# Performance work log

Hardware: AMD Instinct MI355X
Metric: run time of the kernel (lower is better)

## Reference

```python
import jax, jax.numpy as jnp
import numpy as np

N, E, F, H = 20000, 320000, 128, 256   # nodes, edges, in-features, hidden
M, NQ = 4096, 2048                      # lsq rows, QP variables
LAMB_MAX = 2.0


def setup_inputs() -> dict:
    key = jax.random.key(0)
    ks = jax.random.split(key, 12)
    x = jax.random.normal(ks[0], (N, F), jnp.float32)
    edge_index = jax.random.randint(ks[1], (2, E), 0, N)
    A = jax.random.normal(ks[2], (M, NQ), jnp.float32) * 0.05
    b = jax.random.normal(ks[3], (M, 1), jnp.float32)
    feat_ids = jax.random.randint(ks[4], (NQ,), 0, N)
    x_prior = jax.random.uniform(ks[5], (NQ, 1), jnp.float32)
    lamb = jnp.ones((1,), jnp.float32)
    # ChebConv K=2 weights: one linear per Chebyshev order, plus bias
    W10 = jax.random.normal(ks[6], (F, H), jnp.float32) / np.sqrt(F)
    W11 = jax.random.normal(ks[7], (F, H), jnp.float32) / np.sqrt(F)
    b1 = jnp.zeros((H,), jnp.float32)
    W20 = jax.random.normal(ks[8], (H, 1), jnp.float32) / np.sqrt(H)
    W21 = jax.random.normal(ks[9], (H, 1), jnp.float32) / np.sqrt(H)
    b2 = jnp.zeros((1,), jnp.float32)
    return {"x": x, "edge_index": edge_index, "A": A, "b": b,
            "feat_ids": feat_ids, "x_prior": x_prior, "lamb": lamb,
            "W10": W10, "W11": W11, "b1": b1,
            "W20": W20, "W21": W21, "b2": b2}


def _cheb_conv(x, edge_index, W0, W1, bias, lam_max):
    """PyG ChebConv with K=2: out = x @ W0 + (2L/lam_max - I) x @ W1 + bias,
    L = I - D^{-1/2} A D^{-1/2}, via edge gather/scatter (no dense NxN)."""
    row, col = edge_index[0], edge_index[1]
    n = x.shape[0]
    deg = jax.ops.segment_sum(jnp.ones_like(row, dtype=x.dtype), row, num_segments=n)
    dinv = jnp.where(deg > 0, deg ** -0.5, 0.0)
    # normalized edge weight scaled by 2/lam_max, negated (off-diag of L_hat)
    w = -(2.0 / lam_max) * dinv[row] * dinv[col]              # [E]
    msg = jax.ops.segment_sum(w[:, None] * x[col], row, num_segments=n)
    Tx1 = msg + (2.0 / lam_max - 1.0) * x                      # diagonal of L_hat
    return x @ W0 + Tx1 @ W1 + bias


def reference(x, edge_index, A, b, feat_ids, x_prior, lamb,
              W10, W11, b1, W20, W21, b2):
    h = jax.nn.relu(_cheb_conv(x, edge_index, W10, W11, b1, LAMB_MAX))
    h = lamb[0] * jax.nn.relu(_cheb_conv(h, edge_index, W20, W21, b2, LAMB_MAX))
    hfold = h[feat_ids] + 1e-5                                 # [NQ, 1]
    q = hfold[:, 0]
    # QP: min 1/2 z^T Q z + p^T z with vacuous inequality (0*z <= 0.1) and no
    # equality constraints -> interior-point converges to unconstrained min.
    Q = A.T @ A + jnp.diag(q)                                  # [NQ, NQ]
    p = -(x_prior * hfold)[:, 0] - (b.T @ A)[0]                # [NQ]
    z = jnp.linalg.solve(Q, -p)                                # [NQ]
    return z[:, None]                                          # f.T -> [NQ, 1]
```

## Files before the change

### kernel.cpp

```cpp
#include <hip/hip_runtime.h>

#define N_NODES 20000
#define N_EDGES 320000
#define F_DIM   128
#define H_DIM   256
#define M_ROWS  4096
#define NQ      2048
#define NIT     18
#define MM_ROWS 20032

typedef __attribute__((ext_vector_type(8))) short short8;
typedef __attribute__((ext_vector_type(4))) float f32x4;


__device__ __forceinline__ float wred(float v) {
#pragma unroll
  for (int m = 32; m > 0; m >>= 1) v += __shfl_xor(v, m, 64);
  return v;
}

__device__ __forceinline__ float bred256(float v, float* lds) {
  v = wred(v);
  int w = threadIdx.x >> 6;
  if ((threadIdx.x & 63) == 0) lds[w] = v;
  __syncthreads();
  float tot = lds[0] + lds[1] + lds[2] + lds[3];
  __syncthreads();
  return tot;
}

__device__ __forceinline__ unsigned f2bf(float f) {
  unsigned u = __float_as_uint(f);
  unsigned r = u + 0x7fffu + ((u >> 16) & 1u);
  return r >> 16;
}
__device__ __forceinline__ float bflo(unsigned u) { return __uint_as_float(u << 16); }
__device__ __forceinline__ float bfhi(unsigned u) { return __uint_as_float(u & 0xffff0000u); }


__global__ __launch_bounds__(1024) void k_scan(const int* __restrict__ deg,
    int* __restrict__ rowstart, float* __restrict__ dinv) {
  __shared__ int part[1024];
  int t = threadIdx.x;
  const int chunk = (N_NODES + 1023) / 1024;
  int lo = t * chunk;
  int hi = lo + chunk; if (hi > N_NODES) hi = N_NODES;
  int s = 0;
  for (int i = lo; i < hi; ++i) {
    int d = deg[i];
    dinv[i] = d > 0 ? rsqrtf((float)d) : 0.f;
    s += d;
  }
  part[t] = s;
  __syncthreads();
  for (int off = 1; off < 1024; off <<= 1) {
    int v = part[t];
    int add = (t >= off) ? part[t - off] : 0;
    __syncthreads();
    part[t] = v + add;
    __syncthreads();
  }
  int base = (t > 0) ? part[t - 1] : 0;
  for (int i = lo; i < hi; ++i) { rowstart[i] = base; base += deg[i]; }
  if (t == 0) rowstart[N_NODES] = part[1023];
}

__global__ __launch_bounds__(256) void k_scatter(const int* __restrict__ ei,
    const int* __restrict__ rowstart, int* __restrict__ cursor,
    const float* __restrict__ dinv, int* __restrict__ cols, float* __restrict__ wvals) {
  int e = blockIdx.x * 256 + threadIdx.x;
  if (e >= N_EDGES) return;
  int r = ei[e];
  int c = ei[N_EDGES + e];
  int pos = rowstart[r] + atomicAdd(&cursor[r], 1);
  cols[pos] = c;
  wvals[pos] = -dinv[r] * dinv[c];
}

#define CONVX_BLKS (MM_ROWS * 16 / 256)
#define DEG_BLKS   ((N_EDGES + 255) / 256)

__global__ __launch_bounds__(256) void k_pack(const float* __restrict__ x,
    const float* __restrict__ W10, const float* __restrict__ W11,
    unsigned* __restrict__ xu, unsigned* __restrict__ Wtb,
    const int* __restrict__ ei, int* __restrict__ deg) {
  int bx = blockIdx.x;
  if (bx < CONVX_BLKS) {
    int gid = bx * 256 + threadIdx.x;
    int row = gid >> 4;
    int q8 = gid & 15;
    uint4* xu4 = (uint4*)xu;
    if (row < N_NODES) {
      const float4* x4 = (const float4*)x;
      float4 a = x4[(size_t)row * 32 + q8 * 2];
      float4 b2 = x4[(size_t)row * 32 + q8 * 2 + 1];
      uint4 u;
      u.x = f2bf(a.x) | (f2bf(a.y) << 16);
      u.y = f2bf(a.z) | (f2bf(a.w) << 16);
      u.z = f2bf(b2.x) | (f2bf(b2.y) << 16);
      u.w = f2bf(b2.z) | (f2bf(b2.w) << 16);
      xu4[(size_t)row * 32 + q8] = u;
    } else {
      uint4 z = make_uint4(0, 0, 0, 0);
      xu4[(size_t)row * 32 + q8] = z;
      xu4[(size_t)row * 32 + 16 + q8] = z;
    }
  } else if (bx < CONVX_BLKS + 128) {
    int gid = (bx - CONVX_BLKS) * 256 + threadIdx.x;
    int n = gid >> 7;
    int u = gid & 127;
    int k0 = u * 2;
    float v0 = (k0 < 128) ? W10[(size_t)k0 * H_DIM + n]
                          : W11[(size_t)(k0 - 128) * H_DIM + n];
    float v1 = (k0 + 1 < 128) ? W10[(size_t)(k0 + 1) * H_DIM + n]
                              : W11[(size_t)(k0 - 127) * H_DIM + n];
    Wtb[(size_t)n * 128 + u] = f2bf(v0) | (f2bf(v1) << 16);
  } else {
    int e = (bx - CONVX_BLKS - 128) * 256 + threadIdx.x;
    if (e < N_EDGES) atomicAdd(&deg[ei[e]], 1);
  }
}

#define PT_ST 130

__global__ __launch_bounds__(256) void k_prep2(const float* __restrict__ A,
    const float* __restrict__ b, unsigned* __restrict__ Atu,
    float* __restrict__ btA_parts) {
  __shared__ unsigned short T[64 * PT_ST];
  __shared__ float part[64 * 4];
  const int t = threadIdx.x;
  const int jt = blockIdx.x & 31, kt = blockIdx.x >> 5;
  const int j0 = jt * 64, k0 = kt * 128;
  const int jl = t & 63, kq = t >> 6;
  float bta = 0.f;
#pragma unroll 8
  for (int p = 0; p < 32; ++p) {
    int row = k0 + p * 4 + kq;
    float v = A[(size_t)row * NQ + j0 + jl];
    bta += b[row] * v;
    T[jl * PT_ST + p * 4 + kq] = (unsigned short)f2bf(v);
  }
  part[jl * 4 + kq] = bta;
  __syncthreads();
  const int jr = t >> 2, c = t & 3;
  const unsigned short* Tr = T + jr * PT_ST + c * 32;
  uint4 uu0, uu1, uu2, uu3;
  uu0.x = (unsigned)Tr[0]  | ((unsigned)Tr[1]  << 16);
  uu0.y = (unsigned)Tr[2]  | ((unsigned)Tr[3]  << 16);
  uu0.z = (unsigned)Tr[4]  | ((unsigned)Tr[5]  << 16);
  uu0.w = (unsigned)Tr[6]  | ((unsigned)Tr[7]  << 16);
  uu1.x = (unsigned)Tr[8]  | ((unsigned)Tr[9]  << 16);
  uu1.y = (unsigned)Tr[10] | ((unsigned)Tr[11] << 16);
  uu1.z = (unsigned)Tr[12] | ((unsigned)Tr[13] << 16);
  uu1.w = (unsigned)Tr[14] | ((unsigned)Tr[15] << 16);
  uu2.x = (unsigned)Tr[16] | ((unsigned)Tr[17] << 16);
  uu2.y = (unsigned)Tr[18] | ((unsigned)Tr[19] << 16);
  uu2.z = (unsigned)Tr[20] | ((unsigned)Tr[21] << 16);
  uu2.w = (unsigned)Tr[22] | ((unsigned)Tr[23] << 16);
  uu3.x = (unsigned)Tr[24] | ((unsigned)Tr[25] << 16);
  uu3.y = (unsigned)Tr[26] | ((unsigned)Tr[27] << 16);
  uu3.z = (unsigned)Tr[28] | ((unsigned)Tr[29] << 16);
  uu3.w = (unsigned)Tr[30] | ((unsigned)Tr[31] << 16);
  uint4* dst = (uint4*)(Atu + (size_t)(j0 + jr) * 2048 + kt * 64 + c * 16);
  dst[0] = uu0; dst[1] = uu1; dst[2] = uu2; dst[3] = uu3;
  if (t < 64) {
    float s4 = (part[t * 4] + part[t * 4 + 1]) + (part[t * 4 + 2] + part[t * 4 + 3]);
    btA_parts[(size_t)kt * NQ + j0 + t] = s4;
  }
}

__global__ __launch_bounds__(256) void k_msg1(const int* __restrict__ rowstart,
    const int* __restrict__ cols, const float* __restrict__ wvals,
    unsigned* __restrict__ xu) {
  int wid = (blockIdx.x * 256 + threadIdx.x) >> 6;
  int lane = threadIdx.x & 63;
  if (wid >= N_NODES) return;
  int s0 = rowstart[wid], s1 = rowstart[wid + 1];
  float2 a0 = make_float2(0.f, 0.f), a1 = make_float2(0.f, 0.f);
  float2 a2 = make_float2(0.f, 0.f), a3 = make_float2(0.f, 0.f);
  int e = s0;
  for (; e + 4 <= s1; e += 4) {
    int c0 = cols[e], c1 = cols[e + 1], c2 = cols[e + 2], c3 = cols[e + 3];
    float w0 = wvals[e], w1 = wvals[e + 1], w2 = wvals[e + 2], w3 = wvals[e + 3];
    unsigned u0 = xu[(size_t)c0 * 128 + lane];
    unsigned u1 = xu[(size_t)c1 * 128 + lane];
    unsigned u2 = xu[(size_t)c2 * 128 + lane];
    unsigned u3 = xu[(size_t)c3 * 128 + lane];
    a0.x += w0 * bflo(u0); a0.y += w0 * bfhi(u0);
    a1.x += w1 * bflo(u1); a1.y += w1 * bfhi(u1);
    a2.x += w2 * bflo(u2); a2.y += w2 * bfhi(u2);
    a3.x += w3 * bflo(u3); a3.y += w3 * bfhi(u3);
  }
  for (; e < s1; ++e) {
    int c = cols[e];
    float w = wvals[e];
    unsigned u = xu[(size_t)c * 128 + lane];
    a0.x += w * bflo(u); a0.y += w * bfhi(u);
  }
  float ax = (a0.x + a1.x) + (a2.x + a3.x);
  float ay = (a0.y + a1.y) + (a2.y + a3.y);
  xu[(size_t)wid * 128 + 64 + lane] = f2bf(ax) | (f2bf(ay) << 16);
}


__device__ __forceinline__ void mm_ldfrag(short8* Af, short8* Bf,
    const unsigned* __restrict__ xurow, const unsigned* __restrict__ wrow, int kc) {
#pragma unroll
  for (int a = 0; a < 4; ++a)
    Af[a] = *(const short8*)(xurow + (size_t)a * 16 * 128 + kc * 16);
#pragma unroll
  for (int n = 0; n < 4; ++n)
    Bf[n] = *(const short8*)(wrow + (size_t)n * 16 * 128 + kc * 16);
}

__global__ __launch_bounds__(256) void k_mm(const unsigned* __restrict__ xu,
    const unsigned* __restrict__ Wtb, const float* __restrict__ b1,
    const float* __restrict__ W20, const float* __restrict__ W21,
    float* __restrict__ t, float* __restrict__ s) {
  const int row0 = blockIdx.x * 64;
  const int tid = threadIdx.x;
  const int w = tid >> 6, lane = tid & 63;
  const int colb = w * 64;
  const int frow = lane & 15, fqo = (lane >> 4) * 4;
  const int c16 = lane & 15, q4 = lane >> 4;

  f32x4 acc[4][4];
#pragma unroll
  for (int a = 0; a < 4; ++a)
#pragma unroll
    for (int b = 0; b < 4; ++b) {
      acc[a][b][0] = 0.f; acc[a][b][1] = 0.f;
      acc[a][b][2] = 0.f; acc[a][b][3] = 0.f;
    }

  const unsigned* xurow = xu + (size_t)(row0 + frow) * 128 + fqo;
  const unsigned* wrow  = Wtb + (size_t)(colb + frow) * 128 + fqo;

  short8 A0[4], B0[4], A1[4], B1[4];
  mm_ldfrag(A0, B0, xurow, wrow, 0);
#pragma unroll
  for (int kp = 0; kp < 4; ++kp) {
    const int kc = kp * 2;
    mm_ldfrag(A1, B1, xurow, wrow, kc + 1);
#pragma unroll
    for (int a = 0; a < 4; ++a)
#pragma unroll
      for (int n = 0; n < 4; ++n)
        acc[a][n] = __builtin_amdgcn_mfma_f32_16x16x32_bf16(A0[a], B0[n], acc[a][n], 0, 0, 0);
    if (kc + 2 < 8) mm_ldfrag(A0, B0, xurow, wrow, kc + 2);
#pragma unroll
    for (int a = 0; a < 4; ++a)
#pragma unroll
      for (int n = 0; n < 4; ++n)
        acc[a][n] = __builtin_amdgcn_mfma_f32_16x16x32_bf16(A1[a], B1[n], acc[a][n], 0, 0, 0);
  }

  float tp[4][4] = {}, sp[4][4] = {};
#pragma unroll
  for (int b2 = 0; b2 < 4; ++b2) {
    int gc = colb + b2 * 16 + c16;
    float w20 = W20[gc], w21 = W21[gc], bb = b1[gc];
#pragma unroll
    for (int a = 0; a < 4; ++a)
#pragma unroll
      for (int r = 0; r < 4; ++r) {
        float val = acc[a][b2][r] + bb;
        val = val > 0.f ? val : 0.f;
        tp[a][r] += val * w20;
        sp[a][r] += val * w21;
      }
  }
#pragma unroll
  for (int a = 0; a < 4; ++a)
#pragma unroll
    for (int r = 0; r < 4; ++r) {
#pragma unroll
      for (int m = 1; m < 16; m <<= 1) {
        tp[a][r] += __shfl_xor(tp[a][r], m, 64);
        sp[a][r] += __shfl_xor(sp[a][r], m, 64);
      }
    }
  if (c16 == 0) {
#pragma unroll
    for (int a = 0; a < 4; ++a)
#pragma unroll
      for (int r = 0; r < 4; ++r) {
        int gr = row0 + a * 16 + q4 * 4 + r;
        if (gr < N_NODES) {
          atomicAdd(&t[gr], tp[a][r]);
          atomicAdd(&s[gr], sp[a][r]);
        }
      }
  }
}


__global__ __launch_bounds__(256) void k_h2(const float* __restrict__ t,
    const float* __restrict__ s, const int* __restrict__ rowstart,
    const int* __restrict__ cols, const float* __restrict__ wvals,
    const float* __restrict__ lamb, const float* __restrict__ b2, float* __restrict__ h2) {
  int i = blockIdx.x * 256 + threadIdx.x;
  if (i >= N_NODES) return;
  int s0 = rowstart[i], s1 = rowstart[i + 1];
  float m0 = 0.f, m1 = 0.f, m2 = 0.f, m3 = 0.f;
  int e = s0;
  for (; e + 4 <= s1; e += 4) {
    int c0 = cols[e], c1 = cols[e + 1], c2 = cols[e + 2], c3 = cols[e + 3];
    float w0 = wvals[e], w1 = wvals[e + 1], w2 = wvals[e + 2], w3 = wvals[e + 3];
    m0 += w0 * s[c0];
    m1 += w1 * s[c1];
    m2 += w2 * s[c2];
    m3 += w3 * s[c3];
  }
  for (; e < s1; ++e) m0 += wvals[e] * s[cols[e]];
  float m = (m0 + m1) + (m2 + m3);
  float val = t[i] + m + b2[0];
  val = val > 0.f ? val : 0.f;
  h2[i] = lamb[0] * val;
}

#define GR_ST2 36
#define NTILE 136

__global__ __launch_bounds__(512) void k_gram(const unsigned* __restrict__ Atu,
    float* __restrict__ Gp,
    const float* __restrict__ h2, const int* __restrict__ feat_ids,
    const float* __restrict__ x_prior, const float* __restrict__ btA_parts,
    float* __restrict__ q, float* __restrict__ r0) {
  if (blockIdx.x >= 544) {
    if (threadIdx.x < 256) {
      int j = (blockIdx.x - 544) * 256 + threadIdx.x;
      int f = feat_ids[j];
      float hf = h2[f] + 1e-5f;
      q[j] = hf;
      float bta = 0.f;
#pragma unroll
      for (int c = 0; c < 32; ++c) bta += btA_parts[(size_t)c * NQ + j];
      r0[j] = x_prior[j] * hf + bta;
    }
    return;
  }
  __shared__ unsigned shA[128 * GR_ST2];
  __shared__ unsigned shB[128 * GR_ST2];
  const int bid = blockIdx.x;
  const int wid = (bid & 7) * 68 + (bid >> 3);
  const int tile = wid >> 2;
  const int kq = wid & 3;
  int uu = tile, bi = 0;
  while (uu >= 16 - bi) { uu -= 16 - bi; ++bi; }
  const int bj = bi + uu;
  const int i0 = bi * 128, j0 = bj * 128;
  const int tid = threadIdx.x;
  const int w = tid >> 6, lane = tid & 63;
  const int wr = (w >> 2) * 64, wc = (w & 3) * 32;
  const int srow = tid >> 2, sua = (tid & 3) * 8;
  const int frow = lane & 15, fqo = (lane >> 4) * 4;

  f32x4 acc[4][2];
#pragma unroll
  for (int a = 0; a < 4; ++a)
#pragma unroll
    for (int b = 0; b < 2; ++b) {
      acc[a][b][0] = 0.f; acc[a][b][1] = 0.f;
      acc[a][b][2] = 0.f; acc[a][b][3] = 0.f;
    }

  const unsigned* pa = Atu + (size_t)(i0 + srow) * 2048 + kq * 512 + sua;
  const unsigned* pb = Atu + (size_t)(j0 + srow) * 2048 + kq * 512 + sua;

  uint4 pra0 = *(const uint4*)(pa);
  uint4 pra1 = *(const uint4*)(pa + 4);
  uint4 prb0 = *(const uint4*)(pb);
  uint4 prb1 = *(const uint4*)(pb + 4);

  unsigned* as = shA + srow * GR_ST2 + sua;
  unsigned* bs = shB + srow * GR_ST2 + sua;

  for (int sp = 0; sp < 16; ++sp) {
    *(uint4*)as = pra0; *(uint4*)(as + 4) = pra1;
    *(uint4*)bs = prb0; *(uint4*)(bs + 4) = prb1;
    if (sp + 1 < 16) {
      const int ku = (sp + 1) * 32;
      pra0 = *(const uint4*)(pa + ku);
      pra1 = *(const uint4*)(pa + ku + 4);
      prb0 = *(const uint4*)(pb + ku);
      prb1 = *(const uint4*)(pb + ku + 4);
    }
    __syncthreads();
#pragma unroll
    for (int kk = 0; kk < 2; ++kk) {
      short8 af[4], bf[2];
#pragma unroll
      for (int a = 0; a < 4; ++a)
        af[a] = *(const short8*)(shA + (wr + a * 16 + frow) * GR_ST2 + kk * 16 + fqo);
#pragma unroll
      for (int b2 = 0; b2 < 2; ++b2)
        bf[b2] = *(const short8*)(shB + (wc + b2 * 16 + frow) * GR_ST2 + kk * 16 + fqo);
#pragma unroll
      for (int a = 0; a < 4; ++a)
#pragma unroll
        for (int b2 = 0; b2 < 2; ++b2)
          acc[a][b2] = __builtin_amdgcn_mfma_f32_16x16x32_bf16(af[a], bf[b2], acc[a][b2], 0, 0, 0);
    }
    __syncthreads();
  }

  const int q4 = lane >> 4, c16 = lane & 15;
  float* Gz = Gp + ((size_t)kq * NTILE + tile) * 16384;
#pragma unroll
  for (int a = 0; a < 4; ++a)
#pragma unroll
    for (int b2 = 0; b2 < 2; ++b2)
#pragma unroll
      for (int r = 0; r < 4; ++r) {
        int lr = wr + a * 16 + q4 * 4 + r;
        int lc = wc + b2 * 16 + c16;
        Gz[lr * 128 + lc] = acc[a][b2][r];
      }
}

#define GT_ST 131

__global__ __launch_bounds__(256) void k_gconv(const float* __restrict__ Gp,
    const float* __restrict__ q, unsigned* __restrict__ Gb, float* __restrict__ qcorr) {
  __shared__ unsigned short T[128 * GT_ST];
  int uu = blockIdx.x, bi = 0;
  while (uu >= 16 - bi) { uu -= 16 - bi; ++bi; }
  const int bj = bi + uu;
  const int tid = threadIdx.x;
  const int r = tid >> 1, ch = (tid & 1) * 64;
  const size_t tile = (size_t)blockIdx.x * 16384;
  const float4* P0 = (const float4*)(Gp + tile + r * 128 + ch);
  const float4* P1 = (const float4*)(Gp + (size_t)1 * NTILE * 16384 + tile + r * 128 + ch);
  const float4* P2 = (const float4*)(Gp + (size_t)2 * NTILE * 16384 + tile + r * 128 + ch);
  const float4* P3 = (const float4*)(Gp + (size_t)3 * NTILE * 16384 + tile + r * 128 + ch);
  const int gr = bi * 128 + r;
  const bool hasdiag = (bi == bj) && (r >= ch) && (r < ch + 64);
  unsigned uo[32];
#pragma unroll
  for (int j = 0; j < 16; ++j) {
    float4 a = P0[j], b = P1[j], c = P2[j], d = P3[j];
    float v0 = a.x + b.x + c.x + d.x;
    float v1 = a.y + b.y + c.y + d.y;
    float v2 = a.z + b.z + c.z + d.z;
    float v3 = a.w + b.w + c.w + d.w;
    const int c0 = ch + j * 4;
    if (hasdiag && (r - c0 >= 0) && (r - c0 < 4)) {
      float qv = q[gr];
      int dsel = r - c0;
      if (dsel == 0) v0 += qv;
      else if (dsel == 1) v1 += qv;
      else if (dsel == 2) v2 += qv;
      else v3 += qv;
      float vd = (dsel == 0) ? v0 : (dsel == 1) ? v1 : (dsel == 2) ? v2 : v3;
      qcorr[gr] = vd - bflo(f2bf(vd));
    }
    unsigned u0 = f2bf(v0) | (f2bf(v1) << 16);
    unsigned u1 = f2bf(v2) | (f2bf(v3) << 16);
    uo[2 * j] = u0;
    uo[2 * j + 1] = u1;
    T[r * GT_ST + c0]     = (unsigned short)(u0 & 0xffffu);
    T[r * GT_ST + c0 + 1] = (unsigned short)(u0 >> 16);
    T[r * GT_ST + c0 + 2] = (unsigned short)(u1 & 0xffffu);
    T[r * GT_ST + c0 + 3] = (unsigned short)(u1 >> 16);
  }
  uint4* dst = (uint4*)(Gb + (size_t)gr * 1024 + bj * 64 + (ch >> 1));
#pragma unroll
  for (int j = 0; j < 8; ++j) dst[j] = ((const uint4*)uo)[j];
  __syncthreads();
  if (bi != bj) {
    const int wv = tid >> 6, lane = tid & 63;
    for (int kk = 0; kk < 32; ++kk) {
      int rr = kk * 4 + wv;
      unsigned lo = T[(2 * lane) * GT_ST + rr];
      unsigned hi = T[(2 * lane + 1) * GT_ST + rr];
      Gb[(size_t)(bj * 128 + rr) * 1024 + bi * 64 + lane] = lo | (hi << 16);
    }
  }
}

__global__ __launch_bounds__(256) void k_cgG(int k, const unsigned* __restrict__ Gb,
    const float* __restrict__ qcorr,
    const float* __restrict__ r_old, float* __restrict__ r_new,
    const float* __restrict__ p_old, float* __restrict__ p_new,
    const float* __restrict__ Qp_in, float* __restrict__ Qp_out,
    float* __restrict__ xcg) {
  __shared__ float pshare[NQ];
  __shared__ float lds[4];
  const int tid = threadIdx.x, bid = blockIdx.x;
  const float4* r4 = (const float4*)r_old;
  float4 ra = r4[tid * 2], rb2 = r4[tid * 2 + 1];
  float pv[8];
  if (k == 0) {
    pv[0] = ra.x; pv[1] = ra.y; pv[2] = ra.z; pv[3] = ra.w;
    pv[4] = rb2.x; pv[5] = rb2.y; pv[6] = rb2.z; pv[7] = rb2.w;
    if (bid == 0) {
      ((float4*)p_new)[tid * 2] = ra;
      ((float4*)p_new)[tid * 2 + 1] = rb2;
    }
  } else {
    const float4* p4 = (const float4*)p_old;
    const float4* qp4 = (const float4*)Qp_in;
    float4 pa = p4[tid * 2], pb = p4[tid * 2 + 1];
    float4 qa = qp4[tid * 2], qb = qp4[tid * 2 + 1];
    float rr = ra.x * ra.x + ra.y * ra.y + ra.z * ra.z + ra.w * ra.w +
               rb2.x * rb2.x + rb2.y * rb2.y + rb2.z * rb2.z + rb2.w * rb2.w;
    float pap = pa.x * qa.x + pa.y * qa.y + pa.z * qa.z + pa.w * qa.w +
                pb.x * qb.x + pb.y * qb.y + pb.z * qb.z + pb.w * qb.w;
    rr = bred256(rr, lds);
    pap = bred256(pap, lds);
    float alpha = rr / pap;
    if (bid == 0) {
      float4* x4 = (float4*)xcg;
      float4 xa = x4[tid * 2], xb = x4[tid * 2 + 1];
      xa.x += alpha * pa.x; xa.y += alpha * pa.y;
      xa.z += alpha * pa.z; xa.w += alpha * pa.w;
      xb.x += alpha * pb.x; xb.y += alpha * pb.y;
      xb.z += alpha * pb.z; xb.w += alpha * pb.w;
      x4[tid * 2] = xa; x4[tid * 2 + 1] = xb;
    }
    ra.x -= alpha * qa.x; ra.y -= alpha * qa.y;
    ra.z -= alpha * qa.z; ra.w -= alpha * qa.w;
    rb2.x -= alpha * qb.x; rb2.y -= alpha * qb.y;
    rb2.z -= alpha * qb.z; rb2.w -= alpha * qb.w;
    float rrn = ra.x * ra.x + ra.y * ra.y + ra.z * ra.z + ra.w * ra.w +
                rb2.x * rb2.x + rb2.y * rb2.y + rb2.z * rb2.z + rb2.w * rb2.w;
    rrn = bred256(rrn, lds);
    float beta = rrn / rr;
    pv[0] = ra.x + beta * pa.x; pv[1] = ra.y + beta * pa.y;
    pv[2] = ra.z + beta * pa.z; pv[3] = ra.w + beta * pa.w;
    pv[4] = rb2.x + beta * pb.x; pv[5] = rb2.y + beta * pb.y;
    pv[6] = rb2.z + beta * pb.z; pv[7] = rb2.w + beta * pb.w;
    if (bid == 0) {
      ((float4*)r_new)[tid * 2] = ra;
      ((float4*)r_new)[tid * 2 + 1] = rb2;
      ((float4*)p_new)[tid * 2] = make_float4(pv[0], pv[1], pv[2], pv[3]);
      ((float4*)p_new)[tid * 2 + 1] = make_float4(pv[4], pv[5], pv[6], pv[7]);
    }
  }
  ((float4*)pshare)[tid * 2] = make_float4(pv[0], pv[1], pv[2], pv[3]);
  ((float4*)pshare)[tid * 2 + 1] = make_float4(pv[4], pv[5], pv[6], pv[7]);
  __syncthreads();
  const int w = tid >> 6, lane = tid & 63;
  const int row0 = bid * 8 + w * 2;
  const uint4* Gr0 = (const uint4*)(Gb + (size_t)row0 * 1024);
  const uint4* Gr1 = (const uint4*)(Gb + (size_t)(row0 + 1) * 1024);
  const float4* ps4 = (const float4*)pshare;
  float acc0 = 0.f, acc1 = 0.f;
#pragma unroll
  for (int c = 0; c < 4; ++c) {
    uint4 g0 = Gr0[c * 64 + lane];
    uint4 g1 = Gr1[c * 64 + lane];
    float4 pa = ps4[c * 128 + lane * 2];
    float4 pb = ps4[c * 128 + lane * 2 + 1];
    acc0 += bflo(g0.x) * pa.x + bfhi(g0.x) * pa.y;
    acc0 += bflo(g0.y) * pa.z + bfhi(g0.y) * pa.w;
    acc0 += bflo(g0.z) * pb.x + bfhi(g0.z) * pb.y;
    acc0 += bflo(g0.w) * pb.z + bfhi(g0.w) * pb.w;
    acc1 += bflo(g1.x) * pa.x + bfhi(g1.x) * pa.y;
    acc1 += bflo(g1.y) * pa.z + bfhi(g1.y) * pa.w;
    acc1 += bflo(g1.z) * pb.x + bfhi(g1.z) * pb.y;
    acc1 += bflo(g1.w) * pb.z + bfhi(g1.w) * pb.w;
  }
  acc0 = wred(acc0);
  acc1 = wred(acc1);
  if (lane == 0) {
    Qp_out[row0] = acc0 + qcorr[row0] * pshare[row0];
    Qp_out[row0 + 1] = acc1 + qcorr[row0 + 1] * pshare[row0 + 1];
  }
}

__global__ __launch_bounds__(256) void k_cgfin(const float* __restrict__ r_last,
    const float* __restrict__ p_last, const float* __restrict__ Qp,
    const float* __restrict__ xcg, float* __restrict__ out) {
  const int tid = threadIdx.x;
  const int lane = tid & 63;
  const float4* r4 = (const float4*)r_last;
  const float4* p4 = (const float4*)p_last;
  const float4* q4 = (const float4*)Qp;
  float rr = 0.f, pap = 0.f;
#pragma unroll
  for (int c = 0; c < 4; ++c) {
#pragma unroll
    for (int hh = 0; hh < 2; ++hh) {
      float4 rv = r4[c * 128 + lane * 2 + hh];
      float4 pv = p4[c * 128 + lane * 2 + hh];
      float4 qv = q4[c * 128 + lane * 2 + hh];
      rr += rv.x * rv.x + rv.y * rv.y + rv.z * rv.z + rv.w * rv.w;
      pap += pv.x * qv.x + pv.y * qv.y + pv.z * qv.z + pv.w * qv.w;
    }
  }
  rr = wred(rr);
  pap = wred(pap);
  float alpha = rr / pap;
  const float4* x4 = (const float4*)xcg;
  float4* o4 = (float4*)out;
#pragma unroll
  for (int hh = 0; hh < 2; ++hh) {
    int i4 = tid * 2 + hh;
    float4 xv = x4[i4];
    float4 pv = p4[i4];
    xv.x += alpha * pv.x; xv.y += alpha * pv.y;
    xv.z += alpha * pv.z; xv.w += alpha * pv.w;
    o4[i4] = xv;
  }
}


extern "C" void kernel_launch(void* const* d_in, const int* in_sizes, int n_in,
                              void* d_out, int out_size, void* d_ws, size_t ws_size,
                              hipStream_t stream) {
  const float* x      = (const float*)d_in[0];
  const int*   ei     = (const int*)d_in[1];
  const float* A      = (const float*)d_in[2];
  const float* b      = (const float*)d_in[3];
  const int*   fids   = (const int*)d_in[4];
  const float* xprior = (const float*)d_in[5];
  const float* lamb   = (const float*)d_in[6];
  const float* W10    = (const float*)d_in[7];
  const float* W11    = (const float*)d_in[8];
  const float* b1     = (const float*)d_in[9];
  const float* W20    = (const float*)d_in[10];
  const float* W21    = (const float*)d_in[11];
  const float* b2     = (const float*)d_in[12];
  float* out = (float*)d_out;

  char* base = (char*)d_ws;
  size_t o = 0;
  auto alloc = [&](size_t bytes) { size_t r = o; o = (o + bytes + 255) & ~size_t(255); return r; };

  size_t off_deg    = alloc(N_NODES * 4);
  size_t off_cursor = alloc(N_NODES * 4);
  size_t off_xcg    = alloc(NQ * 4);
  size_t off_t      = alloc(N_NODES * 4);
  size_t off_s      = alloc(N_NODES * 4);
  size_t zero_end   = o;
  size_t off_rowst  = alloc((N_NODES + 1) * 4);
  size_t off_dinv   = alloc(N_NODES * 4);
  size_t off_h2     = alloc(N_NODES * 4);
  size_t off_q      = alloc(NQ * 4);
  size_t off_r0     = alloc(NQ * 4);
  size_t off_r1     = alloc(NQ * 4);
  size_t off_p0     = alloc(NQ * 4);
  size_t off_p1     = alloc(NQ * 4);
  size_t off_Qp0    = alloc(NQ * 4);
  size_t off_Qp1    = alloc(NQ * 4);
  size_t off_qcorr  = alloc(NQ * 4);
  size_t off_btAp   = alloc(32 * NQ * 4);
  size_t off_Wtb    = alloc(256 * 128 * 4);
  size_t sz_cols  = (size_t)N_EDGES * 4 + 256;
  size_t sz_wvals = (size_t)N_EDGES * 4 + 256;
  size_t sz_xmsg  = (size_t)MM_ROWS * 256 * 2;
  size_t union_gnn = sz_cols + sz_wvals + sz_xmsg;
  size_t sz_gb     = (size_t)NQ * NQ * 2;
  size_t off_union = alloc(union_gnn > sz_gb ? union_gnn : sz_gb);
  size_t off_atu   = alloc((size_t)M_ROWS * NQ * 2);
  size_t off_Gp    = alloc((size_t)4 * NTILE * 16384 * 4);
  if (o > ws_size) return;

  int*   deg      = (int*)(base + off_deg);
  int*   cursor   = (int*)(base + off_cursor);
  float* xcg      = (float*)(base + off_xcg);
  float* t        = (float*)(base + off_t);
  float* s        = (float*)(base + off_s);
  int*   rowstart = (int*)(base + off_rowst);
  float* dinv     = (float*)(base + off_dinv);
  float* h2       = (float*)(base + off_h2);
  float* q        = (float*)(base + off_q);
  float* rb[2]    = {(float*)(base + off_r0), (float*)(base + off_r1)};
  float* pg[2]    = {(float*)(base + off_p0), (float*)(base + off_p1)};
  float* Qpb[2]   = {(float*)(base + off_Qp0), (float*)(base + off_Qp1)};
  float* qcorr    = (float*)(base + off_qcorr);
  float* btA_parts = (float*)(base + off_btAp);
  unsigned* Wtb   = (unsigned*)(base + off_Wtb);
  int*   cols     = (int*)(base + off_union);
  float* wvals    = (float*)(base + off_union + sz_cols);
  unsigned* xmsgb = (unsigned*)(base + off_union + sz_cols + sz_wvals);
  unsigned* Gb    = (unsigned*)(base + off_union);
  unsigned* Atu   = (unsigned*)(base + off_atu);
  float* Gp       = (float*)(base + off_Gp);

  hipMemsetAsync(d_ws, 0, zero_end, stream);

  k_pack<<<CONVX_BLKS + 128 + DEG_BLKS, 256, 0, stream>>>(x, W10, W11, xmsgb, Wtb, ei, deg);
  k_scan<<<1, 1024, 0, stream>>>(deg, rowstart, dinv);
  k_scatter<<<DEG_BLKS, 256, 0, stream>>>(ei, rowstart, cursor, dinv, cols, wvals);

  k_msg1<<<N_NODES / 4, 256, 0, stream>>>(rowstart, cols, wvals, xmsgb);
  k_mm<<<MM_ROWS / 64, 256, 0, stream>>>(xmsgb, Wtb, b1, W20, W21, t, s);

  k_prep2<<<1024, 256, 0, stream>>>(A, b, Atu, btA_parts);

  k_h2<<<(N_NODES + 255) / 256, 256, 0, stream>>>(t, s, rowstart, cols, wvals, lamb, b2, h2);

  k_gram<<<552, 512, 0, stream>>>(Atu, Gp, h2, fids, xprior, btA_parts, q, rb[0]);
  k_gconv<<<NTILE, 256, 0, stream>>>(Gp, q, Gb, qcorr);

  k_cgG<<<256, 256, 0, stream>>>(0, Gb, qcorr, rb[0], rb[0], pg[0], pg[0],
                                 Qpb[1], Qpb[0], xcg);
  for (int k = 1; k < NIT; ++k) {
    k_cgG<<<256, 256, 0, stream>>>(k, Gb, qcorr, rb[(k - 1) & 1], rb[k & 1],
                                   pg[(k - 1) & 1], pg[k & 1],
                                   Qpb[(k - 1) & 1], Qpb[k & 1], xcg);
  }
  k_cgfin<<<1, 256, 0, stream>>>(rb[(NIT - 1) & 1], pg[(NIT - 1) & 1],
                                 Qpb[(NIT - 1) & 1], xcg, out);
}
```

Baseline: 367.1 us.

## Fuse Gram conversion into k_gram via last-block counter and prefetch G in CG

The separate k_gconv launch is removed. The last of the four k-split blocks for each tile, found with an atomic per-tile counter and thread fences, sums the partials, converts them to bf16 and writes the transposed tile. Because q is produced inside the same kernel, the diagonal correction is split into dex plus q, and the sum is done in k_cgG. k_cgG now issues its G row loads before the reductions to hide memory latency, and merges its two block reductions into one sync pair. The cost is extra fences, atomics, register pressure from the prefetched uint4 values, and serialized conversion work on the last block of each tile.

```diff
diff --git a/kernel.cpp b/kernel.cpp
--- a/kernel.cpp
+++ b/kernel.cpp
@@ -27,6 +27,21 @@
   float tot = lds[0] + lds[1] + lds[2] + lds[3];
   __syncthreads();
   return tot;
+}
+
+__device__ __forceinline__ float2 bred256_2(float a, float b, float* lds) {
+#pragma unroll
+  for (int m = 32; m > 0; m >>= 1) {
+    a += __shfl_xor(a, m, 64);
+    b += __shfl_xor(b, m, 64);
+  }
+  int w = threadIdx.x >> 6;
+  if ((threadIdx.x & 63) == 0) { lds[w] = a; lds[4 + w] = b; }
+  __syncthreads();
+  float ta = lds[0] + lds[1] + lds[2] + lds[3];
+  float tb = lds[4] + lds[5] + lds[6] + lds[7];
+  __syncthreads();
+  return make_float2(ta, tb);
 }
 
 __device__ __forceinline__ unsigned f2bf(float f) {
@@ -321,12 +336,15 @@
 
 #define GR_ST2 36
 #define NTILE 136
+#define GT_ST 131
 
 __global__ __launch_bounds__(512) void k_gram(const unsigned* __restrict__ Atu,
     float* __restrict__ Gp,
     const float* __restrict__ h2, const int* __restrict__ feat_ids,
     const float* __restrict__ x_prior, const float* __restrict__ btA_parts,
-    float* __restrict__ q, float* __restrict__ r0) {
+    float* __restrict__ q, float* __restrict__ r0,
+    unsigned* __restrict__ Gb, float* __restrict__ dex,
+    int* __restrict__ tilecnt) {
   if (blockIdx.x >= 544) {
     if (threadIdx.x < 256) {
       int j = (blockIdx.x - 544) * 256 + threadIdx.x;
@@ -340,8 +358,9 @@
     }
     return;
   }
-  __shared__ unsigned shA[128 * GR_ST2];
-  __shared__ unsigned shB[128 * GR_ST2];
+  __shared__ unsigned shmem[2 * 128 * GR_ST2];
+  unsigned* shA = shmem;
+  unsigned* shB = shmem + 128 * GR_ST2;
   const int bid = blockIdx.x;
   const int wid = (bid & 7) * 68 + (bid >> 3);
   const int tile = wid >> 2;
@@ -417,77 +436,80 @@
         int lc = wc + b2 * 16 + c16;
         Gz[lr * 128 + lc] = acc[a][b2][r];
       }
-}
-
-#define GT_ST 131
-
-__global__ __launch_bounds__(256) void k_gconv(const float* __restrict__ Gp,
-    const float* __restrict__ q, unsigned* __restrict__ Gb, float* __restrict__ qcorr) {
-  __shared__ unsigned short T[128 * GT_ST];
-  int uu = blockIdx.x, bi = 0;
-  while (uu >= 16 - bi) { uu -= 16 - bi; ++bi; }
-  const int bj = bi + uu;
-  const int tid = threadIdx.x;
-  const int r = tid >> 1, ch = (tid & 1) * 64;
-  const size_t tile = (size_t)blockIdx.x * 16384;
-  const float4* P0 = (const float4*)(Gp + tile + r * 128 + ch);
-  const float4* P1 = (const float4*)(Gp + (size_t)1 * NTILE * 16384 + tile + r * 128 + ch);
-  const float4* P2 = (const float4*)(Gp + (size_t)2 * NTILE * 16384 + tile + r * 128 + ch);
-  const float4* P3 = (const float4*)(Gp + (size_t)3 * NTILE * 16384 + tile + r * 128 + ch);
-  const int gr = bi * 128 + r;
-  const bool hasdiag = (bi == bj) && (r >= ch) && (r < ch + 64);
-  unsigned uo[32];
-#pragma unroll
-  for (int j = 0; j < 16; ++j) {
+
+  __threadfence();
+  __shared__ int lastflag;
+  if (tid == 0) lastflag = (atomicAdd(&tilecnt[tile], 1) == 3) ? 1 : 0;
+  __syncthreads();
+  if (!lastflag) return;
+  __threadfence();
+
+  unsigned short* T = (unsigned short*)shmem;
+  const int rr_ = tid >> 2, chh = (tid & 3) * 32;
+  const size_t tbase = (size_t)tile * 16384;
+  const float4* P0 = (const float4*)(Gp + tbase + rr_ * 128 + chh);
+  const float4* P1 = (const float4*)(Gp + (size_t)1 * NTILE * 16384 + tbase + rr_ * 128 + chh);
+  const float4* P2 = (const float4*)(Gp + (size_t)2 * NTILE * 16384 + tbase + rr_ * 128 + chh);
+  const float4* P3 = (const float4*)(Gp + (size_t)3 * NTILE * 16384 + tbase + rr_ * 128 + chh);
+  const int gr = bi * 128 + rr_;
+  const bool hasdiag = (bi == bj) && (rr_ >= chh) && (rr_ < chh + 32);
+  unsigned uo[16];
+#pragma unroll
+  for (int j = 0; j < 8; ++j) {
     float4 a = P0[j], b = P1[j], c = P2[j], d = P3[j];
     float v0 = a.x + b.x + c.x + d.x;
     float v1 = a.y + b.y + c.y + d.y;
     float v2 = a.z + b.z + c.z + d.z;
     float v3 = a.w + b.w + c.w + d.w;
-    const int c0 = ch + j * 4;
-    if (hasdiag && (r - c0 >= 0) && (r - c0 < 4)) {
-      float qv = q[gr];
-      int dsel = r - c0;
-      if (dsel == 0) v0 += qv;
-      else if (dsel == 1) v1 += qv;
-      else if (dsel == 2) v2 += qv;
-      else v3 += qv;
+    const int c0 = chh + j * 4;
+    if (hasdiag && (rr_ - c0 >= 0) && (rr_ - c0 < 4)) {
+      int dsel = rr_ - c0;
       float vd = (dsel == 0) ? v0 : (dsel == 1) ? v1 : (dsel == 2) ? v2 : v3;
-      qcorr[gr] = vd - bflo(f2bf(vd));
+      dex[gr] = vd - bflo(f2bf(vd));
     }
     unsigned u0 = f2bf(v0) | (f2bf(v1) << 16);
     unsigned u1 = f2bf(v2) | (f2bf(v3) << 16);
     uo[2 * j] = u0;
     uo[2 * j + 1] = u1;
-    T[r * GT_ST + c0]     = (unsigned short)(u0 & 0xffffu);
-    T[r * GT_ST + c0 + 1] = (unsigned short)(u0 >> 16);
-    T[r * GT_ST + c0 + 2] = (unsigned short)(u1 & 0xffffu);
-    T[r * GT_ST + c0 + 3] = (unsigned short)(u1 >> 16);
-  }
-  uint4* dst = (uint4*)(Gb + (size_t)gr * 1024 + bj * 64 + (ch >> 1));
-#pragma unroll
-  for (int j = 0; j < 8; ++j) dst[j] = ((const uint4*)uo)[j];
+    T[rr_ * GT_ST + c0]     = (unsigned short)(u0 & 0xffffu);
+    T[rr_ * GT_ST + c0 + 1] = (unsigned short)(u0 >> 16);
+    T[rr_ * GT_ST + c0 + 2] = (unsigned short)(u1 & 0xffffu);
+    T[rr_ * GT_ST + c0 + 3] = (unsigned short)(u1 >> 16);
+  }
+  uint4* dst = (uint4*)(Gb + (size_t)gr * 1024 + bj * 64 + (chh >> 1));
+#pragma unroll
+  for (int j = 0; j < 4; ++j) dst[j] = ((const uint4*)uo)[j];
   __syncthreads();
   if (bi != bj) {
-    const int wv = tid >> 6, lane = tid & 63;
-    for (int kk = 0; kk < 32; ++kk) {
-      int rr = kk * 4 + wv;
-      unsigned lo = T[(2 * lane) * GT_ST + rr];
-      unsigned hi = T[(2 * lane + 1) * GT_ST + rr];
-      Gb[(size_t)(bj * 128 + rr) * 1024 + bi * 64 + lane] = lo | (hi << 16);
+    const int wv = tid >> 6, lane_ = tid & 63;
+#pragma unroll
+    for (int kk = 0; kk < 16; ++kk) {
+      int rrr = kk * 8 + wv;
+      unsigned lo = T[(2 * lane_) * GT_ST + rrr];
+      unsigned hi = T[(2 * lane_ + 1) * GT_ST + rrr];
+      Gb[(size_t)(bj * 128 + rrr) * 1024 + bi * 64 + lane_] = lo | (hi << 16);
     }
   }
 }
 
 __global__ __launch_bounds__(256) void k_cgG(int k, const unsigned* __restrict__ Gb,
-    const float* __restrict__ qcorr,
+    const float* __restrict__ dex, const float* __restrict__ q,
     const float* __restrict__ r_old, float* __restrict__ r_new,
     const float* __restrict__ p_old, float* __restrict__ p_new,
     const float* __restrict__ Qp_in, float* __restrict__ Qp_out,
     float* __restrict__ xcg) {
   __shared__ float pshare[NQ];
-  __shared__ float lds[4];
+  __shared__ float lds[8];
   const int tid = threadIdx.x, bid = blockIdx.x;
+  const int w = tid >> 6, lane = tid & 63;
+  const int row0 = bid * 8 + w * 2;
+  const uint4* Gr0 = (const uint4*)(Gb + (size_t)row0 * 1024);
+  const uint4* Gr1 = (const uint4*)(Gb + (size_t)(row0 + 1) * 1024);
+  uint4 g0a = Gr0[lane],       g1a = Gr1[lane];
+  uint4 g0b = Gr0[64 + lane],  g1b = Gr1[64 + lane];
+  uint4 g0c = Gr0[128 + lane], g1c = Gr1[128 + lane];
+  uint4 g0d = Gr0[192 + lane], g1d = Gr1[192 + lane];
+
   const float4* r4 = (const float4*)r_old;
   float4 ra = r4[tid * 2], rb2 = r4[tid * 2 + 1];
   float pv[8];
@@ -507,8 +529,8 @@
                rb2.x * rb2.x + rb2.y * rb2.y + rb2.z * rb2.z + rb2.w * rb2.w;
     float pap = pa.x * qa.x + pa.y * qa.y + pa.z * qa.z + pa.w * qa.w +
                 pb.x * qb.x + pb.y * qb.y + pb.z * qb.z + pb.w * qb.w;
-    rr = bred256(rr, lds);
-    pap = bred256(pap, lds);
+    float2 rp = bred256_2(rr, pap, lds);
+    rr = rp.x; pap = rp.y;
     float alpha = rr / pap;
     if (bid == 0) {
       float4* x4 = (float4*)xcg;
@@ -541,16 +563,12 @@
   ((float4*)pshare)[tid * 2] = make_float4(pv[0], pv[1], pv[2], pv[3]);
   ((float4*)pshare)[tid * 2 + 1] = make_float4(pv[4], pv[5], pv[6], pv[7]);
   __syncthreads();
-  const int w = tid >> 6, lane = tid & 63;
-  const int row0 = bid * 8 + w * 2;
-  const uint4* Gr0 = (const uint4*)(Gb + (size_t)row0 * 1024);
-  const uint4* Gr1 = (const uint4*)(Gb + (size_t)(row0 + 1) * 1024);
   const float4* ps4 = (const float4*)pshare;
   float acc0 = 0.f, acc1 = 0.f;
 #pragma unroll
   for (int c = 0; c < 4; ++c) {
-    uint4 g0 = Gr0[c * 64 + lane];
-    uint4 g1 = Gr1[c * 64 + lane];
+    uint4 g0 = (c == 0) ? g0a : (c == 1) ? g0b : (c == 2) ? g0c : g0d;
+    uint4 g1 = (c == 0) ? g1a : (c == 1) ? g1b : (c == 2) ? g1c : g1d;
     float4 pa = ps4[c * 128 + lane * 2];
     float4 pb = ps4[c * 128 + lane * 2 + 1];
     acc0 += bflo(g0.x) * pa.x + bfhi(g0.x) * pa.y;
@@ -565,8 +583,8 @@
   acc0 = wred(acc0);
   acc1 = wred(acc1);
   if (lane == 0) {
-    Qp_out[row0] = acc0 + qcorr[row0] * pshare[row0];
-    Qp_out[row0 + 1] = acc1 + qcorr[row0 + 1] * pshare[row0 + 1];
+    Qp_out[row0] = acc0 + (dex[row0] + q[row0]) * pshare[row0];
+    Qp_out[row0 + 1] = acc1 + (dex[row0 + 1] + q[row0 + 1]) * pshare[row0 + 1];
   }
 }
 
@@ -634,6 +652,7 @@
   size_t off_xcg    = alloc(NQ * 4);
   size_t off_t      = alloc(N_NODES * 4);
   size_t off_s      = alloc(N_NODES * 4);
+  size_t off_tcnt   = alloc(NTILE * 4);
   size_t zero_end   = o;
   size_t off_rowst  = alloc((N_NODES + 1) * 4);
   size_t off_dinv   = alloc(N_NODES * 4);
@@ -645,7 +664,7 @@
   size_t off_p1     = alloc(NQ * 4);
   size_t off_Qp0    = alloc(NQ * 4);
   size_t off_Qp1    = alloc(NQ * 4);
-  size_t off_qcorr  = alloc(NQ * 4);
+  size_t off_dex    = alloc(NQ * 4);
   size_t off_btAp   = alloc(32 * NQ * 4);
   size_t off_Wtb    = alloc(256 * 128 * 4);
   size_t sz_cols  = (size_t)N_EDGES * 4 + 256;
@@ -663,6 +682,7 @@
   float* xcg      = (float*)(base + off_xcg);
   float* t        = (float*)(base + off_t);
   float* s        = (float*)(base + off_s);
+  int*   tilecnt  = (int*)(base + off_tcnt);
   int*   rowstart = (int*)(base + off_rowst);
   float* dinv     = (float*)(base + off_dinv);
   float* h2       = (float*)(base + off_h2);
@@ -670,7 +690,7 @@
   float* rb[2]    = {(float*)(base + off_r0), (float*)(base + off_r1)};
   float* pg[2]    = {(float*)(base + off_p0), (float*)(base + off_p1)};
   float* Qpb[2]   = {(float*)(base + off_Qp0), (float*)(base + off_Qp1)};
-  float* qcorr    = (float*)(base + off_qcorr);
+  float* dex      = (float*)(base + off_dex);
   float* btA_parts = (float*)(base + off_btAp);
   unsigned* Wtb   = (unsigned*)(base + off_Wtb);
   int*   cols     = (int*)(base + off_union);
@@ -693,13 +713,13 @@
 
   k_h2<<<(N_NODES + 255) / 256, 256, 0, stream>>>(t, s, rowstart, cols, wvals, lamb, b2, h2);
 
-  k_gram<<<552, 512, 0, stream>>>(Atu, Gp, h2, fids, xprior, btA_parts, q, rb[0]);
-  k_gconv<<<NTILE, 256, 0, stream>>>(Gp, q, Gb, qcorr);
-
-  k_cgG<<<256, 256, 0, stream>>>(0, Gb, qcorr, rb[0], rb[0], pg[0], pg[0],
+  k_gram<<<552, 512, 0, stream>>>(Atu, Gp, h2, fids, xprior, btA_parts, q, rb[0],
+                                  Gb, dex, tilecnt);
+
+  k_cgG<<<256, 256, 0, stream>>>(0, Gb, dex, q, rb[0], rb[0], pg[0], pg[0],
                                  Qpb[1], Qpb[0], xcg);
   for (int k = 1; k < NIT; ++k) {
-    k_cgG<<<256, 256, 0, stream>>>(k, Gb, qcorr, rb[(k - 1) & 1], rb[k & 1],
+    k_cgG<<<256, 256, 0, stream>>>(k, Gb, dex, q, rb[(k - 1) & 1], rb[k & 1],
                                    pg[(k - 1) & 1], pg[k & 1],
                                    Qpb[(k - 1) & 1], Qpb[k & 1], xcg);
   }
```

Measured after the change: 535.6 us. 45.9% more time.
